# Kernel tuning notes

Measured on AMD Instinct MI355X. Metric: run time of the kernel, lower is better.

## Reference

```python
import jax, jax.numpy as jnp
import numpy as np

N_QUBITS = 8
DEPTH = 2
INPUT_DIM = 128
HIDDEN = 128
SEQ = 128
BATCH = 512
DIM = 2 ** N_QUBITS

# Z expectation signs: wire 0 is the most-significant qubit of the state index.
_bits = (np.arange(DIM)[None, :] >> (N_QUBITS - 1 - np.arange(N_QUBITS)[:, None])) & 1
Z_SIGNS = jnp.asarray(1.0 - 2.0 * _bits, dtype=jnp.float32)  # [n_wires, DIM]


def _apply_1q(state, mat, wire):
    """Apply a 2x2 gate on `wire`. mat: [2,2] or batched [bsz,2,2]."""
    bsz = state.shape[0]
    st = state.reshape(bsz, 2 ** wire, 2, -1)
    if mat.ndim == 3:
        out = jnp.einsum('bij,bxjy->bxiy', mat, st)
    else:
        out = jnp.einsum('ij,bxjy->bxiy', mat, st)
    return out.reshape(bsz, DIM)


def _rx_mat(theta):  # theta: [bsz] -> [bsz,2,2] complex
    c = jnp.cos(theta * 0.5).astype(jnp.complex64)
    s = ((-1j) * jnp.sin(theta * 0.5)).astype(jnp.complex64)
    return jnp.stack([jnp.stack([c, s], -1), jnp.stack([s, c], -1)], -2)


def _ry_mat(theta):  # scalar theta -> [2,2] complex
    c = jnp.cos(theta * 0.5)
    s = jnp.sin(theta * 0.5)
    return jnp.stack([jnp.stack([c, -s]), jnp.stack([s, c])]).astype(jnp.complex64)


def _cnot_adj(state, wire):
    """CNOT control=wire, target=wire+1 (adjacent wires)."""
    bsz = state.shape[0]
    st = state.reshape(bsz, 2 ** wire, 4, -1)
    st = st[:, :, jnp.array([0, 1, 3, 2]), :]  # |10>-><|11| swap
    return st.reshape(bsz, DIM)


def _qgate(q_in, params):
    """Variational circuit: RX encoding (first N_QUBITS features of q_in),
    DEPTH x (RY layer + CNOT chain), measure Z on each wire."""
    bsz = q_in.shape[0]
    state = jnp.zeros((bsz, DIM), jnp.complex64).at[:, 0].set(1.0)
    for w in range(N_QUBITS):
        state = _apply_1q(state, _rx_mat(q_in[:, w]), w)
    for d in range(DEPTH):
        for w in range(N_QUBITS):
            state = _apply_1q(state, _ry_mat(params[d, w]), w)
        for w in range(N_QUBITS - 1):
            state = _cnot_adj(state, w)
    probs = state.real ** 2 + state.imag ** 2  # [bsz, DIM]
    return probs @ Z_SIGNS.T  # [bsz, n_wires]


def setup_inputs() -> dict:
    key = jax.random.key(0)
    ks = jax.random.split(key, 16)
    d_in = INPUT_DIM + HIDDEN
    inv = 1.0 / jnp.sqrt(jnp.float32(d_in))
    invq = 1.0 / jnp.sqrt(jnp.float32(N_QUBITS))
    return {
        'inputs': jax.random.normal(ks[0], (SEQ, BATCH, INPUT_DIM), jnp.float32),
        'Wq': jax.random.normal(ks[1], (4 * N_QUBITS, d_in), jnp.float32) * inv,
        'bq': jnp.zeros((4 * N_QUBITS,), jnp.float32),
        'pf': jax.random.normal(ks[2], (DEPTH, N_QUBITS), jnp.float32),
        'pi': jax.random.normal(ks[3], (DEPTH, N_QUBITS), jnp.float32),
        'pg': jax.random.normal(ks[4], (DEPTH, N_QUBITS), jnp.float32),
        'po': jax.random.normal(ks[5], (DEPTH, N_QUBITS), jnp.float32),
        'Wf': jax.random.normal(ks[6], (HIDDEN, N_QUBITS), jnp.float32) * invq,
        'bf': jnp.zeros((HIDDEN,), jnp.float32),
        'Wi': jax.random.normal(ks[7], (HIDDEN, N_QUBITS), jnp.float32) * invq,
        'bi': jnp.zeros((HIDDEN,), jnp.float32),
        'Wg': jax.random.normal(ks[8], (HIDDEN, N_QUBITS), jnp.float32) * invq,
        'bg': jnp.zeros((HIDDEN,), jnp.float32),
        'Wo': jax.random.normal(ks[9], (HIDDEN, N_QUBITS), jnp.float32) * invq,
        'bo': jnp.zeros((HIDDEN,), jnp.float32),
    }


def reference(inputs, Wq, bq, pf, pi, pg, po, Wf, bf, Wi, bi, Wg, bg, Wo, bo):
    bsz = inputs.shape[1]
    h0 = jnp.zeros((bsz, HIDDEN), jnp.float32)
    c0 = jnp.zeros((bsz, HIDDEN), jnp.float32)

    def step(carry, x):
        hx, cx = carry
        combined = jnp.concatenate([x, hx], axis=1)
        q_in = combined @ Wq.T + bq  # [bsz, 4*n_qubits]; only first n_qubits used per gate
        f = jax.nn.sigmoid(_qgate(q_in, pf) @ Wf.T + bf)
        i = jax.nn.sigmoid(_qgate(q_in, pi) @ Wi.T + bi)
        g = jnp.tanh(_qgate(q_in, pg) @ Wg.T + bg)
        o = jax.nn.sigmoid(_qgate(q_in, po) @ Wo.T + bo)
        cx_new = f * cx + i * g
        hx_new = o * jnp.tanh(cx_new)
        return (hx_new, cx_new), hx_new

    (hx, cx), outputs = jax.lax.scan(step, (h0, c0), inputs)
    return outputs, hx, cx
```

## Files before the change

### kernel.cpp

```cpp
#include <hip/hip_runtime.h>

#define SEQ 128
#define BATCH 512
#define IN_DIM 128
#define HID 128

typedef float vf2 __attribute__((ext_vector_type(2)));

#define LOG2E 1.4426950408889634f
#define INV2PI 0.15915494309189535f

__device__ __forceinline__ float rcp_f(float x) { return __builtin_amdgcn_rcpf(x); }
__device__ __forceinline__ float exp2_f(float x) { float r; asm("v_exp_f32 %0, %1" : "=v"(r) : "v"(x)); return r; }
__device__ __forceinline__ float sin2pi_f(float x) { float r; asm("v_sin_f32 %0, %1" : "=v"(r) : "v"(x)); return r; }
__device__ __forceinline__ float cos2pi_f(float x) { float r; asm("v_cos_f32 %0, %1" : "=v"(r) : "v"(x)); return r; }
__device__ __forceinline__ float tanh_f(float x) {
  return 1.0f - 2.0f * rcp_f(exp2_f(x * 2.885390082f) + 1.0f);
}

template <int CTRL>
__device__ __forceinline__ float dpp_add(float s) {
  return s + __int_as_float(__builtin_amdgcn_mov_dpp(__float_as_int(s), CTRL, 0xF, 0xF, true));
}
__device__ __forceinline__ float rdlane(float v, int src) {
  return __int_as_float(__builtin_amdgcn_readlane(__float_as_int(v), src));
}

__global__ __launch_bounds__(64) void qlstm_kernel(
    const float* __restrict__ X, const float* __restrict__ Wq, const float* __restrict__ bq,
    const float* __restrict__ pf, const float* __restrict__ pi_, const float* __restrict__ pg,
    const float* __restrict__ po, const float* __restrict__ Wf, const float* __restrict__ bf,
    const float* __restrict__ Wi, const float* __restrict__ bi, const float* __restrict__ Wg,
    const float* __restrict__ bg, const float* __restrict__ Wo, const float* __restrict__ bo,
    float* __restrict__ out)
{
  __shared__ __align__(16) float h_sw[160];
  __shared__ __align__(16) float gsh[4 * HID];

  const int lane = threadIdx.x;
  const int r = lane >> 3, c = lane & 7;
  const int g = lane >> 4, p = lane & 15;
  const int b = blockIdx.x;
  const int D0 = 2 * lane;

  const float* gW = (g == 0) ? Wf : (g == 1) ? Wi : (g == 2) ? Wg : Wo;
  const float* gB = (g == 0) ? bf : (g == 1) ? bi : (g == 2) ? bg : bo;
  const float* gP = (g == 0) ? pf : (g == 1) ? pi_ : (g == 2) ? pg : po;

  vf2 wx[8], wh[8];
  {
    const vf2* pxw = (const vf2*)(Wq + r * 256 + 16 * c);
    const vf2* phw = (const vf2*)(Wq + r * 256 + 128 + 16 * c);
#pragma unroll
    for (int j = 0; j < 8; ++j) { wx[j] = pxw[j] * INV2PI; wh[j] = phw[j] * INV2PI; }
  }
  const float bqv = bq[r] * INV2PI;

  const float amul = (g == 2) ? 2.0f : 1.0f;
  const float oadd = (g == 2) ? -1.0f : 0.0f;
  const float ksc  = -amul * LOG2E;

  vf2 wg2[8][4];
#pragma unroll
  for (int w = 0; w < 8; ++w)
#pragma unroll
    for (int j = 0; j < 4; ++j) {
      wg2[w][j].x = gW[(8 * p + 2 * j)     * 8 + w] * ksc;
      wg2[w][j].y = gW[(8 * p + 2 * j + 1) * 8 + w] * ksc;
    }
  vf2 bias2[4];
#pragma unroll
  for (int j = 0; j < 4; ++j) {
    bias2[j].x = gB[8 * p + 2 * j]     * ksc;
    bias2[j].y = gB[8 * p + 2 * j + 1] * ksc;
  }
  vf2 cbsb[8]; float C1[8], S1[8];
#pragma unroll
  for (int w = 0; w < 8; ++w) {
    float th0 = gP[w], th1 = gP[8 + w];
    cbsb[w].x = cosf(th0); cbsb[w].y = sinf(th0);
    C1[w] = cosf(th1); S1[w] = sinf(th1);
  }

  vf2 c2; c2.x = 0.f; c2.y = 0.f;
  vf2 h2v; h2v.x = 0.f; h2v.y = 0.f;
  float4 hh0 = {0,0,0,0}, hh1 = {0,0,0,0}, hh2 = {0,0,0,0}, hh3 = {0,0,0,0};

  const float* xg = X + (size_t)b * IN_DIM + 16 * c;
  float* outp = out + (size_t)b * HID + D0;
  char* hb    = (char*)h_sw + 80 * c;
  char* hwp   = (char*)h_sw + 80 * (D0 >> 4) + 4 * (D0 & 15);

  float xp_cur;
  float4 xA0, xA1, xA2, xA3, xB0, xB1, xB2, xB3;
  {
    const float4* x0_ = (const float4*)xg;
    float4 a0 = x0_[0], a1 = x0_[1], a2 = x0_[2], a3 = x0_[3];
    vf2 t0 = wx[0] * (vf2){a0.x, a0.y} + wx[1] * (vf2){a0.z, a0.w};
    vf2 t1 = wx[2] * (vf2){a1.x, a1.y} + wx[3] * (vf2){a1.z, a1.w};
    vf2 t2 = wx[4] * (vf2){a2.x, a2.y} + wx[5] * (vf2){a2.z, a2.w};
    vf2 t3 = wx[6] * (vf2){a3.x, a3.y} + wx[7] * (vf2){a3.z, a3.w};
    vf2 ax = (t0 + t1) + (t2 + t3);
    xp_cur = ax.x + ax.y;
    const float4* x1_ = (const float4*)(xg + (size_t)1 * (BATCH * IN_DIM));
    xA0 = x1_[0]; xA1 = x1_[1]; xA2 = x1_[2]; xA3 = x1_[3];
  }

#define QSTEP(XC0, XC1, XC2, XC3, XL0, XL1, XL2, XL3, T)                              \
  {                                                                                   \
          \
    {                                                                                 \
      const int tl_ = ((T) + 2 < SEQ) ? (T) + 2 : (SEQ - 1);                          \
      const float4* xn_ = (const float4*)(xg + (size_t)tl_ * (BATCH * IN_DIM));       \
      XL0 = xn_[0]; XL1 = xn_[1]; XL2 = xn_[2]; XL3 = xn_[3];                         \
    }                                                                                 \
                  \
    float zz;                                                                         \
    {                                                                                 \
      vf2 t0 = wh[0] * (vf2){hh0.x, hh0.y} + wh[1] * (vf2){hh0.z, hh0.w};             \
      vf2 t1 = wh[2] * (vf2){hh1.x, hh1.y} + wh[3] * (vf2){hh1.z, hh1.w};             \
      vf2 t2 = wh[4] * (vf2){hh2.x, hh2.y} + wh[5] * (vf2){hh2.z, hh2.w};             \
      vf2 t3 = wh[6] * (vf2){hh3.x, hh3.y} + wh[7] * (vf2){hh3.z, hh3.w};             \
      vf2 aq = ((t0 + t1) + (t2 + t3)) + (vf2){xp_cur, 0.0f};                         \
      float s_ = aq.x + aq.y;                                                         \
      s_ = dpp_add<0xB1>(s_); s_ = dpp_add<0x4E>(s_); s_ = dpp_add<0x141>(s_);        \
      zz = s_ + bqv;                                      \
    }                                                                                 \
    float szv = sin2pi_f(zz), czv = cos2pi_f(zz);                                     \
               \
    float cqs[8], sqs[8];                                                             \
    _Pragma("unroll")                                                                 \
    for (int w = 0; w < 8; ++w) { cqs[w] = rdlane(czv, 8 * w); sqs[w] = rdlane(szv, 8 * w); } \
                   \
    vf2 acc0 = bias2[0], acc1 = bias2[1], acc2 = bias2[2], acc3 = bias2[3];           \
    float u_, d_, P_, R_;                                                             \
    {                                                                                 \
      vf2 KA0 = cbsb[0] * cqs[0];                                                     \
      u_ = C1[0]; d_ = C1[0] * KA0.x;                                                 \
      P_ = -S1[0] * KA0.y; R_ = -S1[0] * sqs[0];                                      \
    }                                                                                 \
    _Pragma("unroll")                                                                 \
    for (int w = 1; w < 8; ++w) {                                                     \
      vf2 KA = cbsb[w] * cqs[w];                                                      \
      float K_ = KA.x, A2_ = KA.y, B2_ = sqs[w];                                      \
      float Md = fmaf(A2_, P_, d_);                                                   \
      float MP = fmaf(A2_, d_, P_);                                                   \
      float Mu = fmaf(K_, u_, -(B2_ * R_));                                           \
      float MR = fmaf(B2_, u_, K_ * R_);                                              \
      acc0 += Md * wg2[w - 1][0]; acc1 += Md * wg2[w - 1][1];                         \
      acc2 += Md * wg2[w - 1][2]; acc3 += Md * wg2[w - 1][3];                         \
      u_ = C1[w] * Md; d_ = C1[w] * Mu;                                               \
      P_ = -S1[w] * MP; R_ = -S1[w] * MR;                                             \
    }                                                                                 \
    float ev7_ = d_ + P_;                                                             \
    acc0 += ev7_ * wg2[7][0]; acc1 += ev7_ * wg2[7][1];                               \
    acc2 += ev7_ * wg2[7][2]; acc3 += ev7_ * wg2[7][3];                               \
                  \
    float av_[8] = {acc0.x, acc0.y, acc1.x, acc1.y, acc2.x, acc2.y, acc3.x, acc3.y};  \
    float o8[8];                                                                      \
    _Pragma("unroll")                                                                 \
    for (int k = 0; k < 8; ++k) {                                                     \
      float e_ = exp2_f(av_[k]);                                                      \
      o8[k] = fmaf(rcp_f(1.0f + e_), amul, oadd);                                     \
    }                                                                                 \
        \
    {                                                                                 \
      float4* gp4 = (float4*)(gsh + g * HID + 8 * p);                                 \
      float4 w0; w0.x = o8[0]; w0.y = o8[1]; w0.z = o8[2]; w0.w = o8[3];              \
      float4 w1; w1.x = o8[4]; w1.y = o8[5]; w1.z = o8[6]; w1.w = o8[7];              \
      gp4[0] = w0; gp4[1] = w1;                                                       \
    }                                                                                 \
    vf2 fv = *(const vf2*)(gsh + 0 * HID + D0);                                       \
    vf2 iv = *(const vf2*)(gsh + 1 * HID + D0);                                       \
    vf2 gv = *(const vf2*)(gsh + 2 * HID + D0);                                       \
    vf2 ov = *(const vf2*)(gsh + 3 * HID + D0);                                       \
                                        \
    c2 = fv * c2 + iv * gv;                                                           \
    h2v.x = ov.x * tanh_f(c2.x);                                                      \
    h2v.y = ov.y * tanh_f(c2.y);                                                      \
               \
    *(vf2*)hwp = h2v;                                                                 \
    hh0 = *(const float4*)(hb);                                                       \
    hh1 = *(const float4*)(hb + 16);                                                  \
    hh2 = *(const float4*)(hb + 32);                                                  \
    hh3 = *(const float4*)(hb + 48);                                                  \
            \
    {                                                                                 \
      vf2 t0 = wx[0] * (vf2){XC0.x, XC0.y} + wx[1] * (vf2){XC0.z, XC0.w};             \
      vf2 t1 = wx[2] * (vf2){XC1.x, XC1.y} + wx[3] * (vf2){XC1.z, XC1.w};             \
      vf2 t2 = wx[4] * (vf2){XC2.x, XC2.y} + wx[5] * (vf2){XC2.z, XC2.w};             \
      vf2 t3 = wx[6] * (vf2){XC3.x, XC3.y} + wx[7] * (vf2){XC3.z, XC3.w};             \
      vf2 axn = (t0 + t1) + (t2 + t3);                                                \
      xp_cur = axn.x + axn.y;                                                         \
    }                                                                                 \
    *(vf2*)(outp + (size_t)(T) * (BATCH * HID)) = h2v;                                \
  }

#pragma unroll 1
  for (int tt = 0; tt < SEQ; tt += 2) {
    QSTEP(xA0, xA1, xA2, xA3, xB0, xB1, xB2, xB3, tt);
    QSTEP(xB0, xB1, xB2, xB3, xA0, xA1, xA2, xA3, tt + 1);
  }
#undef QSTEP

  {
    size_t base = (size_t)SEQ * BATCH * HID;
    *(vf2*)(out + base + (size_t)b * HID + D0) = h2v;
    *(vf2*)(out + base + (size_t)BATCH * HID + (size_t)b * HID + D0) = c2;
  }
}

extern "C" void kernel_launch(void* const* d_in, const int* in_sizes, int n_in,
                              void* d_out, int out_size, void* d_ws, size_t ws_size,
                              hipStream_t stream) {
  (void)in_sizes; (void)n_in; (void)out_size; (void)d_ws; (void)ws_size;
  const float* X   = (const float*)d_in[0];
  const float* Wq  = (const float*)d_in[1];
  const float* bq  = (const float*)d_in[2];
  const float* pf  = (const float*)d_in[3];
  const float* pi_ = (const float*)d_in[4];
  const float* pg  = (const float*)d_in[5];
  const float* po  = (const float*)d_in[6];
  const float* Wf  = (const float*)d_in[7];
  const float* bf  = (const float*)d_in[8];
  const float* Wi  = (const float*)d_in[9];
  const float* bi  = (const float*)d_in[10];
  const float* Wg  = (const float*)d_in[11];
  const float* bg  = (const float*)d_in[12];
  const float* Wo  = (const float*)d_in[13];
  const float* bo  = (const float*)d_in[14];
  float* out = (float*)d_out;

  qlstm_kernel<<<BATCH, 64, 0, stream>>>(X, Wq, bq, pf, pi_, pg, po,
                                         Wf, bf, Wi, bi, Wg, bg, Wo, bo, out);
}
```

Before: 182.8 us.

## Replace LDS exchange with register-resident cross-lane reductions and DPP gate rotation

Removes the shared-memory buffers for h and the gate outputs. The Wq projection is now computed per lane from that lane's own hidden pair, followed by a butterfly reduction across the wave built from permlane32_swap, ds_swizzle and DPP. The gate matmul rotates the circuit expectation values across quad lanes with DPP, so each lane computes all four gates for its own two hidden units and selects them in registers. This is meant to cut LDS round-trips and their wait latency on the serial per-step critical path, at the cost of more cross-lane shuffles and more VALU selects.

```diff
diff --git a/kernel.cpp b/kernel.cpp
--- a/kernel.cpp
+++ b/kernel.cpp
@@ -22,8 +22,20 @@
 __device__ __forceinline__ float dpp_add(float s) {
   return s + __int_as_float(__builtin_amdgcn_mov_dpp(__float_as_int(s), CTRL, 0xF, 0xF, true));
 }
+template <int CTRL>
+__device__ __forceinline__ float dpp_mov(float s) {
+  return __int_as_float(__builtin_amdgcn_mov_dpp(__float_as_int(s), CTRL, 0xF, 0xF, true));
+}
 __device__ __forceinline__ float rdlane(float v, int src) {
   return __int_as_float(__builtin_amdgcn_readlane(__float_as_int(v), src));
+}
+__device__ __forceinline__ float xor32_sum(float x) {
+  unsigned xu = __float_as_uint(x);
+  auto pr = __builtin_amdgcn_permlane32_swap(xu, xu, false, false);
+  return __uint_as_float(pr[0]) + __uint_as_float(pr[1]);
+}
+__device__ __forceinline__ float swz16(float x) {
+  return __int_as_float(__builtin_amdgcn_ds_swizzle(__float_as_int(x), 0x401F));
 }
 
 __global__ __launch_bounds__(64) void qlstm_kernel(
@@ -34,46 +46,46 @@
     const float* __restrict__ bg, const float* __restrict__ Wo, const float* __restrict__ bo,
     float* __restrict__ out)
 {
-  __shared__ __align__(16) float h_sw[160];
-  __shared__ __align__(16) float gsh[4 * HID];
-
   const int lane = threadIdx.x;
-  const int r = lane >> 3, c = lane & 7;
-  const int g = lane >> 4, p = lane & 15;
+  const int r = lane >> 3;
+  const int q = lane & 3;
+  const bool l3 = (lane >> 3) & 1;
+  const bool l4 = (lane >> 4) & 1;
+  const bool l5 = (lane >> 5) & 1;
+  const bool qb0 = q & 1;
+  const bool qb1 = (q >> 1) & 1;
+  const int D0 = 2 * lane;
   const int b = blockIdx.x;
-  const int D0 = 2 * lane;
-
-  const float* gW = (g == 0) ? Wf : (g == 1) ? Wi : (g == 2) ? Wg : Wo;
-  const float* gB = (g == 0) ? bf : (g == 1) ? bi : (g == 2) ? bg : bo;
-  const float* gP = (g == 0) ? pf : (g == 1) ? pi_ : (g == 2) ? pg : po;
-
-  vf2 wx[8], wh[8];
-  {
-    const vf2* pxw = (const vf2*)(Wq + r * 256 + 16 * c);
-    const vf2* phw = (const vf2*)(Wq + r * 256 + 128 + 16 * c);
-#pragma unroll
-    for (int j = 0; j < 8; ++j) { wx[j] = pxw[j] * INV2PI; wh[j] = phw[j] * INV2PI; }
+
+  float wxx[8], wxy[8], whx[8], why[8];
+#pragma unroll
+  for (int w = 0; w < 8; ++w) {
+    wxx[w] = Wq[w * 256 + D0]       * INV2PI;
+    wxy[w] = Wq[w * 256 + D0 + 1]   * INV2PI;
+    whx[w] = Wq[w * 256 + 128 + D0] * INV2PI;
+    why[w] = Wq[w * 256 + 128 + D0 + 1] * INV2PI;
   }
   const float bqv = bq[r] * INV2PI;
 
-  const float amul = (g == 2) ? 2.0f : 1.0f;
-  const float oadd = (g == 2) ? -1.0f : 0.0f;
-  const float ksc  = -amul * LOG2E;
-
-  vf2 wg2[8][4];
-#pragma unroll
-  for (int w = 0; w < 8; ++w)
-#pragma unroll
-    for (int j = 0; j < 4; ++j) {
-      wg2[w][j].x = gW[(8 * p + 2 * j)     * 8 + w] * ksc;
-      wg2[w][j].y = gW[(8 * p + 2 * j + 1) * 8 + w] * ksc;
+  vf2 wgk[8][4]; vf2 biask[4]; float amulk[4], oaddk[4];
+#pragma unroll
+  for (int k = 0; k < 4; ++k) {
+    const int gk = (q + k) & 3;
+    const float* W = (gk == 0) ? Wf : (gk == 1) ? Wi : (gk == 2) ? Wg : Wo;
+    const float* B = (gk == 0) ? bf : (gk == 1) ? bi : (gk == 2) ? bg : bo;
+    const float am = (gk == 2) ? 2.0f : 1.0f;
+    amulk[k] = am;
+    oaddk[k] = (gk == 2) ? -1.0f : 0.0f;
+    const float ks = -am * LOG2E;
+#pragma unroll
+    for (int w = 0; w < 8; ++w) {
+      wgk[w][k].x = W[D0 * 8 + w] * ks;
+      wgk[w][k].y = W[(D0 + 1) * 8 + w] * ks;
     }
-  vf2 bias2[4];
-#pragma unroll
-  for (int j = 0; j < 4; ++j) {
-    bias2[j].x = gB[8 * p + 2 * j]     * ksc;
-    bias2[j].y = gB[8 * p + 2 * j + 1] * ksc;
-  }
+    biask[k].x = B[D0] * ks;
+    biask[k].y = B[D0 + 1] * ks;
+  }
+  const float* gP = (q == 0) ? pf : (q == 1) ? pi_ : (q == 2) ? pg : po;
   vf2 cbsb[8]; float C1[8], S1[8];
 #pragma unroll
   for (int w = 0; w < 8; ++w) {
@@ -84,55 +96,57 @@
 
   vf2 c2; c2.x = 0.f; c2.y = 0.f;
   vf2 h2v; h2v.x = 0.f; h2v.y = 0.f;
-  float4 hh0 = {0,0,0,0}, hh1 = {0,0,0,0}, hh2 = {0,0,0,0}, hh3 = {0,0,0,0};
-
-  const float* xg = X + (size_t)b * IN_DIM + 16 * c;
+  float xpart[8];
+
+  const float* xgl = X + (size_t)b * IN_DIM + D0;
   float* outp = out + (size_t)b * HID + D0;
-  char* hb    = (char*)h_sw + 80 * c;
-  char* hwp   = (char*)h_sw + 80 * (D0 >> 4) + 4 * (D0 & 15);
-
-  float xp_cur;
-  float4 xA0, xA1, xA2, xA3, xB0, xB1, xB2, xB3;
+
+  vf2 xcA, xcB;
   {
-    const float4* x0_ = (const float4*)xg;
-    float4 a0 = x0_[0], a1 = x0_[1], a2 = x0_[2], a3 = x0_[3];
-    vf2 t0 = wx[0] * (vf2){a0.x, a0.y} + wx[1] * (vf2){a0.z, a0.w};
-    vf2 t1 = wx[2] * (vf2){a1.x, a1.y} + wx[3] * (vf2){a1.z, a1.w};
-    vf2 t2 = wx[4] * (vf2){a2.x, a2.y} + wx[5] * (vf2){a2.z, a2.w};
-    vf2 t3 = wx[6] * (vf2){a3.x, a3.y} + wx[7] * (vf2){a3.z, a3.w};
-    vf2 ax = (t0 + t1) + (t2 + t3);
-    xp_cur = ax.x + ax.y;
-    const float4* x1_ = (const float4*)(xg + (size_t)1 * (BATCH * IN_DIM));
-    xA0 = x1_[0]; xA1 = x1_[1]; xA2 = x1_[2]; xA3 = x1_[3];
-  }
-
-#define QSTEP(XC0, XC1, XC2, XC3, XL0, XL1, XL2, XL3, T)                              \
+    vf2 x0 = *(const vf2*)xgl;
+#pragma unroll
+    for (int w = 0; w < 8; ++w) xpart[w] = fmaf(x0.x, wxx[w], x0.y * wxy[w]);
+    xcA = *(const vf2*)(xgl + (size_t)1 * (BATCH * IN_DIM));
+  }
+
+#define QSTEP(XC, XL, T)                                                              \
   {                                                                                   \
-          \
+           \
     {                                                                                 \
       const int tl_ = ((T) + 2 < SEQ) ? (T) + 2 : (SEQ - 1);                          \
-      const float4* xn_ = (const float4*)(xg + (size_t)tl_ * (BATCH * IN_DIM));       \
-      XL0 = xn_[0]; XL1 = xn_[1]; XL2 = xn_[2]; XL3 = xn_[3];                         \
-    }                                                                                 \
-                  \
-    float zz;                                                                         \
-    {                                                                                 \
-      vf2 t0 = wh[0] * (vf2){hh0.x, hh0.y} + wh[1] * (vf2){hh0.z, hh0.w};             \
-      vf2 t1 = wh[2] * (vf2){hh1.x, hh1.y} + wh[3] * (vf2){hh1.z, hh1.w};             \
-      vf2 t2 = wh[4] * (vf2){hh2.x, hh2.y} + wh[5] * (vf2){hh2.z, hh2.w};             \
-      vf2 t3 = wh[6] * (vf2){hh3.x, hh3.y} + wh[7] * (vf2){hh3.z, hh3.w};             \
-      vf2 aq = ((t0 + t1) + (t2 + t3)) + (vf2){xp_cur, 0.0f};                         \
-      float s_ = aq.x + aq.y;                                                         \
-      s_ = dpp_add<0xB1>(s_); s_ = dpp_add<0x4E>(s_); s_ = dpp_add<0x141>(s_);        \
-      zz = s_ + bqv;                                      \
-    }                                                                                 \
+      XL = *(const vf2*)(xgl + (size_t)tl_ * (BATCH * IN_DIM));                       \
+    }                                                                                 \
+              \
+    float part[8];                                                                    \
+    _Pragma("unroll")                                                                 \
+    for (int w = 0; w < 8; ++w)                                                       \
+      part[w] = fmaf(h2v.x, whx[w], fmaf(h2v.y, why[w], xpart[w]));                   \
+    float tA[8];                                                                      \
+    _Pragma("unroll")                                                                 \
+    for (int w = 0; w < 8; ++w) tA[w] = xor32_sum(part[w]);                \
+    float nB0 = l5 ? tA[4] : tA[0];                                                   \
+    float nB1 = l5 ? tA[5] : tA[1];                                                   \
+    float nB2 = l5 ? tA[6] : tA[2];                                                   \
+    float nB3 = l5 ? tA[7] : tA[3];                                                   \
+    float sB0 = swz16(nB0), sB1 = swz16(nB1), sB2 = swz16(nB2), sB3 = swz16(nB3);     \
+            \
+    _Pragma("unroll")                                                                 \
+    for (int w = 0; w < 8; ++w) xpart[w] = fmaf(XC.x, wxx[w], XC.y * wxy[w]);         \
+    float tB0 = nB0 + sB0, tB1 = nB1 + sB1, tB2 = nB2 + sB2, tB3 = nB3 + sB3;         \
+    float mC0 = l4 ? tB2 : tB0;                                                       \
+    float mC1 = l4 ? tB3 : tB1;                                                       \
+    float tC0 = mC0 + dpp_mov<0x128>(mC0);                                  \
+    float tC1 = mC1 + dpp_mov<0x128>(mC1);                                            \
+    float zr = l3 ? tC1 : tC0;                                                        \
+    zr = dpp_add<0xB1>(zr); zr = dpp_add<0x4E>(zr); zr = dpp_add<0x141>(zr);          \
+    float zz = zr + bqv;                                  \
+                   \
     float szv = sin2pi_f(zz), czv = cos2pi_f(zz);                                     \
-               \
     float cqs[8], sqs[8];                                                             \
     _Pragma("unroll")                                                                 \
     for (int w = 0; w < 8; ++w) { cqs[w] = rdlane(czv, 8 * w); sqs[w] = rdlane(szv, 8 * w); } \
                    \
-    vf2 acc0 = bias2[0], acc1 = bias2[1], acc2 = bias2[2], acc3 = bias2[3];           \
+    vf2 acc0 = biask[0], acc1 = biask[1], acc2 = biask[2], acc3 = biask[3];           \
     float u_, d_, P_, R_;                                                             \
     {                                                                                 \
       vf2 KA0 = cbsb[0] * cqs[0];                                                     \
@@ -147,59 +161,57 @@
       float MP = fmaf(A2_, d_, P_);                                                   \
       float Mu = fmaf(K_, u_, -(B2_ * R_));                                           \
       float MR = fmaf(B2_, u_, K_ * R_);                                              \
-      acc0 += Md * wg2[w - 1][0]; acc1 += Md * wg2[w - 1][1];                         \
-      acc2 += Md * wg2[w - 1][2]; acc3 += Md * wg2[w - 1][3];                         \
+      float e1 = dpp_mov<0x39>(Md);                               \
+      float e2 = dpp_mov<0x4E>(Md);                               \
+      float e3 = dpp_mov<0x93>(Md);                               \
+      acc0 += Md * wgk[w - 1][0];                                                     \
+      acc1 += e1 * wgk[w - 1][1];                                                     \
+      acc2 += e2 * wgk[w - 1][2];                                                     \
+      acc3 += e3 * wgk[w - 1][3];                                                     \
       u_ = C1[w] * Md; d_ = C1[w] * Mu;                                               \
       P_ = -S1[w] * MP; R_ = -S1[w] * MR;                                             \
     }                                                                                 \
-    float ev7_ = d_ + P_;                                                             \
-    acc0 += ev7_ * wg2[7][0]; acc1 += ev7_ * wg2[7][1];                               \
-    acc2 += ev7_ * wg2[7][2]; acc3 += ev7_ * wg2[7][3];                               \
-                  \
-    float av_[8] = {acc0.x, acc0.y, acc1.x, acc1.y, acc2.x, acc2.y, acc3.x, acc3.y};  \
-    float o8[8];                                                                      \
-    _Pragma("unroll")                                                                 \
-    for (int k = 0; k < 8; ++k) {                                                     \
-      float e_ = exp2_f(av_[k]);                                                      \
-      o8[k] = fmaf(rcp_f(1.0f + e_), amul, oadd);                                     \
-    }                                                                                 \
-        \
     {                                                                                 \
-      float4* gp4 = (float4*)(gsh + g * HID + 8 * p);                                 \
-      float4 w0; w0.x = o8[0]; w0.y = o8[1]; w0.z = o8[2]; w0.w = o8[3];              \
-      float4 w1; w1.x = o8[4]; w1.y = o8[5]; w1.z = o8[6]; w1.w = o8[7];              \
-      gp4[0] = w0; gp4[1] = w1;                                                       \
-    }                                                                                 \
-    vf2 fv = *(const vf2*)(gsh + 0 * HID + D0);                                       \
-    vf2 iv = *(const vf2*)(gsh + 1 * HID + D0);                                       \
-    vf2 gv = *(const vf2*)(gsh + 2 * HID + D0);                                       \
-    vf2 ov = *(const vf2*)(gsh + 3 * HID + D0);                                       \
-                                        \
+      float ev7_ = d_ + P_;                                                           \
+      float e1 = dpp_mov<0x39>(ev7_);                                                 \
+      float e2 = dpp_mov<0x4E>(ev7_);                                                 \
+      float e3 = dpp_mov<0x93>(ev7_);                                                 \
+      acc0 += ev7_ * wgk[7][0];                                                       \
+      acc1 += e1 * wgk[7][1];                                                         \
+      acc2 += e2 * wgk[7][2];                                                         \
+      acc3 += e3 * wgk[7][3];                                                         \
+    }                                                                                 \
+               \
+    vf2 av0, av1, av2, av3;                                                           \
+    av0.x = fmaf(rcp_f(1.0f + exp2_f(acc0.x)), amulk[0], oaddk[0]);                   \
+    av0.y = fmaf(rcp_f(1.0f + exp2_f(acc0.y)), amulk[0], oaddk[0]);                   \
+    av1.x = fmaf(rcp_f(1.0f + exp2_f(acc1.x)), amulk[1], oaddk[1]);                   \
+    av1.y = fmaf(rcp_f(1.0f + exp2_f(acc1.y)), amulk[1], oaddk[1]);                   \
+    av2.x = fmaf(rcp_f(1.0f + exp2_f(acc2.x)), amulk[2], oaddk[2]);                   \
+    av2.y = fmaf(rcp_f(1.0f + exp2_f(acc2.y)), amulk[2], oaddk[2]);                   \
+    av3.x = fmaf(rcp_f(1.0f + exp2_f(acc3.x)), amulk[3], oaddk[3]);                   \
+    av3.y = fmaf(rcp_f(1.0f + exp2_f(acc3.y)), amulk[3], oaddk[3]);                   \
+                \
+    vf2 b0 = qb0 ? av3 : av0;                                                         \
+    vf2 b1 = qb0 ? av0 : av1;                                                         \
+    vf2 b2 = qb0 ? av1 : av2;                                                         \
+    vf2 b3 = qb0 ? av2 : av3;                                                         \
+    vf2 fv = qb1 ? b2 : b0;                                                           \
+    vf2 iv = qb1 ? b3 : b1;                                                           \
+    vf2 gv = qb1 ? b0 : b2;                                                           \
+    vf2 ov = qb1 ? b1 : b3;                                                           \
+                            \
     c2 = fv * c2 + iv * gv;                                                           \
     h2v.x = ov.x * tanh_f(c2.x);                                                      \
     h2v.y = ov.y * tanh_f(c2.y);                                                      \
-               \
-    *(vf2*)hwp = h2v;                                                                 \
-    hh0 = *(const float4*)(hb);                                                       \
-    hh1 = *(const float4*)(hb + 16);                                                  \
-    hh2 = *(const float4*)(hb + 32);                                                  \
-    hh3 = *(const float4*)(hb + 48);                                                  \
-            \
-    {                                                                                 \
-      vf2 t0 = wx[0] * (vf2){XC0.x, XC0.y} + wx[1] * (vf2){XC0.z, XC0.w};             \
-      vf2 t1 = wx[2] * (vf2){XC1.x, XC1.y} + wx[3] * (vf2){XC1.z, XC1.w};             \
-      vf2 t2 = wx[4] * (vf2){XC2.x, XC2.y} + wx[5] * (vf2){XC2.z, XC2.w};             \
-      vf2 t3 = wx[6] * (vf2){XC3.x, XC3.y} + wx[7] * (vf2){XC3.z, XC3.w};             \
-      vf2 axn = (t0 + t1) + (t2 + t3);                                                \
-      xp_cur = axn.x + axn.y;                                                         \
-    }                                                                                 \
+                                                       \
     *(vf2*)(outp + (size_t)(T) * (BATCH * HID)) = h2v;                                \
   }
 
 #pragma unroll 1
   for (int tt = 0; tt < SEQ; tt += 2) {
-    QSTEP(xA0, xA1, xA2, xA3, xB0, xB1, xB2, xB3, tt);
-    QSTEP(xB0, xB1, xB2, xB3, xA0, xA1, xA2, xA3, tt + 1);
+    QSTEP(xcA, xcB, tt);
+    QSTEP(xcB, xcA, tt + 1);
   }
 #undef QSTEP
 
```

New measurement: 186.0 us. Within noise of the previous version (+1.7%).
